# Performance work log

Measured on AMD Instinct MI355X. Metric: run time of the kernel, lower is better.

Reference implementation:

```python
import jax, jax.numpy as jnp
import numpy as np

SCALE = 1.0 / np.sqrt(512.0).astype(np.float32)  # attention() hardcodes d_k=512


def setup_inputs() -> dict:
    key = jax.random.key(0)
    ks = jax.random.split(key, 9)
    B, S, D = 4, 2048, 512
    mk = lambda k, shape: jax.random.normal(k, shape, dtype=jnp.float32) * 0.05
    return {
        "q": mk(ks[0], (B, S, D)),
        "k": mk(ks[1], (B, S, D)),
        "v": mk(ks[2], (B, S, D)),
        "WQ_w": mk(ks[3], (D, D)),
        "WQ_b": mk(ks[4], (D,)),
        "WK_w": mk(ks[5], (D, D)),
        "WK_b": mk(ks[6], (D,)),
        "WV_w": mk(ks[7], (D, D)),
        "WV_b": mk(ks[8], (D,)),
    }


def reference(q, k, v, WQ_w, WQ_b, WK_w, WK_b, WV_w, WV_b):
    # torch nn.Linear: y = x @ W.T + b
    qp = q @ WQ_w.T + WQ_b  # [B,S,dk]
    kp = k @ WK_w.T + WK_b  # [B,S,dk]
    vp = v @ WV_w.T + WV_b  # [B,S,dv]
    qk = jnp.einsum("bqd,bkd->bqk", qp, kp) * SCALE  # [B,Sq,Sk]
    S = qk.shape[1]
    tril = jnp.tril(jnp.ones((S, S), dtype=qk.dtype))  # multiplicative causal mask
    qk = qk * tril
    # NOTE: original applies softmax over dim=1 (the query axis), faithfully kept.
    attn = jax.nn.softmax(qk, axis=1)
    out = jnp.einsum("bqk,bkd->bqd", attn, vp)  # [B,Sq,dv]
    return out
```

## Files before the change

### kernel.cpp

```cpp
#include <hip/hip_runtime.h>
#include <hip/hip_bf16.h>


#define S_LEN 2048
#define D_DIM 512
#define SCALE_F 0.044194173824159216f

typedef __attribute__((ext_vector_type(8))) short s8v;
typedef __attribute__((ext_vector_type(4))) short s4v;
typedef __attribute__((ext_vector_type(4))) float f4v;

enum { EPI_BIAS = 0, EPI_BIAS_T = 1, EPI_SCORES = 2 };

__device__ __forceinline__ short f2bf_s(float f) {
  union { __hip_bfloat16 b; short s; } u; u.b = __float2bfloat16(f); return u.s;
}
__device__ __forceinline__ float bf2f_s(short h) {
  union { short s; __hip_bfloat16 b; } u; u.s = h; return __bfloat162float(u.b);
}

__device__ __forceinline__ void glds16(const short* g, short* l) {
  __builtin_amdgcn_global_load_lds((const __attribute__((address_space(1))) void*)g,
                                   (__attribute__((address_space(3))) void*)l, 16, 0, 0);
}

template <int EPI>
__device__ __forceinline__ void gemm_core(
    const short* __restrict__ A, const short* __restrict__ B,
    short* __restrict__ C, const float* __restrict__ bias,
    short* SMEM, int N, int K, size_t sCz, int m0, int n0, int bz,
    float* __restrict__ Z)
{
  short* As = SMEM;
  short* Bs = SMEM + 8192;

  const int tid  = threadIdx.x;
  const int w    = tid >> 6;
  const int lane = tid & 63;
  const int quad = lane >> 4;
  const int l16  = lane & 15;
  const int wm   = (w >> 1) * 64;
  const int wn   = (w & 1) * 64;

  const int strow = tid >> 3;
  const int gl = ((tid & 7) ^ (strow & 7)) * 8;

  f4v acc[4][4];
#pragma unroll
  for (int i = 0; i < 4; ++i)
#pragma unroll
    for (int j = 0; j < 4; ++j)
#pragma unroll
      for (int r = 0; r < 4; ++r) acc[i][j][r] = 0.0f;

  const short* Ag = A + (size_t)(m0 + strow) * K + gl;
  const short* Bg = B + (size_t)(n0 + strow) * K + gl;
  short* Asl = As + tid * 8;
  short* Bsl = Bs + tid * 8;
  const size_t pstr = (size_t)32 * K;

  const int swq = l16 & 7;

  for (int k0 = 0; k0 < K; k0 += 64) {
#pragma unroll
    for (int p = 0; p < 4; ++p) glds16(Ag + k0 + p * pstr, Asl + p * 2048);
#pragma unroll
    for (int p = 0; p < 4; ++p) glds16(Bg + k0 + p * pstr, Bsl + p * 2048);
    __syncthreads();

#pragma unroll
    for (int kk = 0; kk < 2; ++kk) {
      s8v af[4], bf[4];
#pragma unroll
      for (int i = 0; i < 4; ++i)
        af[i] = *(const s8v*)&As[(wm + i * 16 + l16) * 64 + (((kk * 4 + quad) ^ swq) * 8)];
#pragma unroll
      for (int j = 0; j < 4; ++j)
        bf[j] = *(const s8v*)&Bs[(wn + j * 16 + l16) * 64 + (((kk * 4 + quad) ^ swq) * 8)];
#pragma unroll
      for (int i = 0; i < 4; ++i)
#pragma unroll
        for (int j = 0; j < 4; ++j)
          acc[i][j] = __builtin_amdgcn_mfma_f32_16x16x32_bf16(af[i], bf[j], acc[i][j], 0, 0, 0);
    }
    __syncthreads();
  }

  float bv[4];
  if (EPI == EPI_BIAS || EPI == EPI_BIAS_T) {
#pragma unroll
    for (int j = 0; j < 4; ++j) bv[j] = bias[n0 + wn + j * 16 + l16];
  }

  if (EPI == EPI_BIAS_T) {
#pragma unroll
    for (int i = 0; i < 4; ++i) {
#pragma unroll
      for (int j = 0; j < 4; ++j) {
        const int gn  = n0 + wn + j * 16 + l16;
        const int gmb = m0 + wm + i * 16 + quad * 4;
        const int bb = gmb >> 11, ssb = gmb & (S_LEN - 1);
        s4v o;
#pragma unroll
        for (int r = 0; r < 4; ++r) o[r] = f2bf_s(acc[i][j][r] + bv[j]);
        *(s4v*)&C[((size_t)bb * D_DIM + gn) * S_LEN + ssb] = o;
      }
    }
    return;
  }

  short* TB = SMEM;
  const int wbase = w * 2176;
  float csum[4] = {0.f, 0.f, 0.f, 0.f};

#pragma unroll
  for (int ph = 0; ph < 2; ++ph) {
    __syncthreads();
#pragma unroll
    for (int ii = 0; ii < 2; ++ii) {
      const int i = ph * 2 + ii;
#pragma unroll
      for (int j = 0; j < 4; ++j) {
        const int gn = n0 + wn + j * 16 + l16;
#pragma unroll
        for (int r = 0; r < 4; ++r) {
          short o;
          if (EPI == EPI_SCORES) {
            const int gm = m0 + wm + i * 16 + quad * 4 + r;
            const float e = (gm >= gn) ? __expf(acc[i][j][r] * SCALE_F) : 1.0f;
            csum[j] += e;
            o = f2bf_s(e);
          } else {
            o = f2bf_s(acc[i][j][r] + bv[j]);
          }
          TB[wbase + (ii * 16 + quad * 4 + r) * 68 + j * 16 + l16] = o;
        }
      }
    }
    __syncthreads();
#pragma unroll
    for (int p = 0; p < 4; ++p) {
      const int row = p * 8 + (lane >> 3);
      const int cg  = lane & 7;
      const s8v vv = *(const s8v*)&TB[wbase + row * 68 + cg * 8];
      const int gm = m0 + wm + ph * 32 + row;
      const int gn = n0 + wn + cg * 8;
      *(s8v*)&C[sCz + (size_t)gm * N + gn] = vv;
    }
  }

  if (EPI == EPI_SCORES) {
#pragma unroll
    for (int j = 0; j < 4; ++j) {
      float cs = csum[j];
      cs += __shfl_xor(cs, 16, 64);
      cs += __shfl_xor(cs, 32, 64);
      if (quad == 0) atomicAdd(&Z[(bz << 11) + n0 + wn + j * 16 + l16], cs);
    }
  }
}

__global__ __launch_bounds__(256, 2) void gemm_scores(
    const short* __restrict__ A, const short* __restrict__ B, short* __restrict__ C,
    float* __restrict__ Z)
{
  __shared__ __align__(16) short SMEM[16384];
  const int bz = blockIdx.z;
  gemm_core<EPI_SCORES>(A + (size_t)bz * S_LEN * D_DIM, B + (size_t)bz * S_LEN * D_DIM,
                        C, nullptr, SMEM, S_LEN, D_DIM,
                        (size_t)bz * S_LEN * S_LEN, blockIdx.y * 128, blockIdx.x * 128,
                        bz, Z);
}

__global__ __launch_bounds__(256, 2) void proj3(
    const short* __restrict__ a0, const short* __restrict__ a1, const short* __restrict__ a2,
    const short* __restrict__ b0, const short* __restrict__ b1, const short* __restrict__ b2,
    short* __restrict__ c0, short* __restrict__ c1, short* __restrict__ c2,
    const float* __restrict__ x0, const float* __restrict__ x1, const float* __restrict__ x2)
{
  __shared__ __align__(16) short SMEM[16384];
  const int z = blockIdx.z;
  const short* A = (z == 0) ? a0 : (z == 1) ? a1 : a2;
  const short* B = (z == 0) ? b0 : (z == 1) ? b1 : b2;
  short*       C = (z == 0) ? c0 : (z == 1) ? c1 : c2;
  const float* bias = (z == 0) ? x0 : (z == 1) ? x1 : x2;
  if (z == 2)
    gemm_core<EPI_BIAS_T>(A, B, C, bias, SMEM, D_DIM, D_DIM, 0,
                          blockIdx.y * 128, blockIdx.x * 128, 0, nullptr);
  else
    gemm_core<EPI_BIAS>(A, B, C, bias, SMEM, D_DIM, D_DIM, 0,
                        blockIdx.y * 128, blockIdx.x * 128, 0, nullptr);
}

__global__ __launch_bounds__(256, 2) void gemm_out(
    const short* __restrict__ E, const short* __restrict__ vpT,
    float* __restrict__ out)
{
  __shared__ __align__(16) short As[64 * 64];
  __shared__ __align__(16) short Bs[128 * 64];

  const int tid  = threadIdx.x;
  const int bz   = blockIdx.z;
  const int m0   = blockIdx.y * 64;
  const int n0   = blockIdx.x * 128;

  const short* A = E   + (size_t)bz * S_LEN * S_LEN;
  const short* B = vpT + (size_t)bz * D_DIM * S_LEN;

  const int w    = tid >> 6;
  const int lane = tid & 63;
  const int quad = lane >> 4;
  const int l16  = lane & 15;
  const int wm   = (w >> 1) * 32;
  const int wn   = (w & 1) * 64;

  const int strow = tid >> 3;
  const int gl = ((tid & 7) ^ (strow & 7)) * 8;

  f4v acc[2][4];
#pragma unroll
  for (int i = 0; i < 2; ++i)
#pragma unroll
    for (int j = 0; j < 4; ++j)
#pragma unroll
      for (int r = 0; r < 4; ++r) acc[i][j][r] = 0.0f;

  const short* Ag = A + (size_t)(m0 + strow) * S_LEN + gl;
  const short* Bg = B + (size_t)(n0 + strow) * S_LEN + gl;
  short* Asl = As + tid * 8;
  short* Bsl = Bs + tid * 8;
  const size_t pstr = (size_t)32 * S_LEN;

  const int swq = l16 & 7;

  for (int k0 = 0; k0 < S_LEN; k0 += 64) {
#pragma unroll
    for (int p = 0; p < 2; ++p) glds16(Ag + k0 + p * pstr, Asl + p * 2048);
#pragma unroll
    for (int p = 0; p < 4; ++p) glds16(Bg + k0 + p * pstr, Bsl + p * 2048);
    __syncthreads();

#pragma unroll
    for (int kk = 0; kk < 2; ++kk) {
      s8v af[2], bf[4];
#pragma unroll
      for (int i = 0; i < 2; ++i)
        af[i] = *(const s8v*)&As[(wm + i * 16 + l16) * 64 + (((kk * 4 + quad) ^ swq) * 8)];
#pragma unroll
      for (int j = 0; j < 4; ++j)
        bf[j] = *(const s8v*)&Bs[(wn + j * 16 + l16) * 64 + (((kk * 4 + quad) ^ swq) * 8)];
#pragma unroll
      for (int i = 0; i < 2; ++i)
#pragma unroll
        for (int j = 0; j < 4; ++j)
          acc[i][j] = __builtin_amdgcn_mfma_f32_16x16x32_bf16(af[i], bf[j], acc[i][j], 0, 0, 0);
    }
    __syncthreads();
  }

  float* Cf = out + (size_t)bz * S_LEN * D_DIM;
#pragma unroll
  for (int i = 0; i < 2; ++i) {
#pragma unroll
    for (int j = 0; j < 4; ++j) {
      const int gn = n0 + wn + j * 16 + l16;
#pragma unroll
      for (int r = 0; r < 4; ++r) {
        const int gm = m0 + wm + i * 16 + quad * 4 + r;
        Cf[(size_t)gm * D_DIM + gn] = acc[i][j][r];
      }
    }
  }
}

__global__ __launch_bounds__(256) void cvt3(
    const float* __restrict__ s0, const float* __restrict__ s1,
    const float* __restrict__ s2, short* __restrict__ dst, int n)
{
  const float* s = (blockIdx.y == 0) ? s0 : (blockIdx.y == 1) ? s1 : s2;
  short* d = dst + (size_t)blockIdx.y * n;
  const int i = (blockIdx.x * 256 + threadIdx.x) * 8;
  if (i >= n) return;
  const float4 f0 = *(const float4*)(s + i);
  const float4 f1 = *(const float4*)(s + i + 4);
  s8v o;
  o[0] = f2bf_s(f0.x); o[1] = f2bf_s(f0.y); o[2] = f2bf_s(f0.z); o[3] = f2bf_s(f0.w);
  o[4] = f2bf_s(f1.x); o[5] = f2bf_s(f1.y); o[6] = f2bf_s(f1.z); o[7] = f2bf_s(f1.w);
  *(s8v*)(d + i) = o;
}

__global__ __launch_bounds__(256) void scale_vpt(
    short* __restrict__ vpT, const float* __restrict__ Z)
{
  const size_t base = ((size_t)blockIdx.x * 256 + threadIdx.x) * 8;
  const int kk = (int)(base & (S_LEN - 1));
  const int b  = (int)(base >> 20);
  const float4 z0 = *(const float4*)&Z[(b << 11) + kk];
  const float4 z1 = *(const float4*)&Z[(b << 11) + kk + 4];
  s8v v = *(s8v*)&vpT[base];
  v[0] = f2bf_s(bf2f_s(v[0]) / z0.x); v[1] = f2bf_s(bf2f_s(v[1]) / z0.y);
  v[2] = f2bf_s(bf2f_s(v[2]) / z0.z); v[3] = f2bf_s(bf2f_s(v[3]) / z0.w);
  v[4] = f2bf_s(bf2f_s(v[4]) / z1.x); v[5] = f2bf_s(bf2f_s(v[5]) / z1.y);
  v[6] = f2bf_s(bf2f_s(v[6]) / z1.z); v[7] = f2bf_s(bf2f_s(v[7]) / z1.w);
  *(s8v*)&vpT[base] = v;
}

extern "C" void kernel_launch(void* const* d_in, const int* in_sizes, int n_in,
                              void* d_out, int out_size, void* d_ws, size_t ws_size,
                              hipStream_t stream) {
  const float* q   = (const float*)d_in[0];
  const float* k   = (const float*)d_in[1];
  const float* v   = (const float*)d_in[2];
  const float* WQw = (const float*)d_in[3];
  const float* WQb = (const float*)d_in[4];
  const float* WKw = (const float*)d_in[5];
  const float* WKb = (const float*)d_in[6];
  const float* WVw = (const float*)d_in[7];
  const float* WVb = (const float*)d_in[8];

  char* ws = (char*)d_ws;
  short* E   = (short*)(ws);
  short* qb  = (short*)(ws);
  short* Wqb = (short*)(ws + 25165824);
  short* qp  = (short*)(ws + 33554432);
  short* kp  = (short*)(ws + 41943040);
  short* vpT = (short*)(ws + 50331648);
  float* Z   = (float*)(ws + 58720256);
  short* kb  = qb + 4194304;
  short* vb  = qb + 8388608;
  short* Wkb = Wqb + 262144;
  short* Wvb = Wqb + 524288;

  const dim3 blk(256);

  hipMemsetAsync(Z, 0, 4 * S_LEN * sizeof(float), stream);

  cvt3<<<dim3(2048, 3), blk, 0, stream>>>(q, k, v, qb, 4194304);
  cvt3<<<dim3(128, 3), blk, 0, stream>>>(WQw, WKw, WVw, Wqb, 262144);

  proj3<<<dim3(4, 64, 3), blk, 0, stream>>>(
      qb, kb, vb, Wqb, Wkb, Wvb, qp, kp, vpT, WQb, WKb, WVb);

  gemm_scores<<<dim3(16, 16, 4), blk, 0, stream>>>(qp, kp, E, Z);

  scale_vpt<<<dim3(2048), blk, 0, stream>>>(vpT, Z);

  gemm_out<<<dim3(4, 32, 4), blk, 0, stream>>>(E, vpT, (float*)d_out);
}
```

Before: 202.8 us.

## Multi-buffer LDS tiles to overlap global loads with MFMA in GEMM kernels

Replaces the single-buffered load/sync/compute loop with a double-buffered pipeline in the shared GEMM core (scores and projections) and a triple-buffered pipeline in the output GEMM. Loads for the next tile are issued before computing the current one, with explicit vmcnt waits and raw s_barrier in place of __syncthreads. The aim is to hide global-to-LDS latency behind MFMA work. The cost is double or more LDS per block, which can reduce occupancy, and the hand-written waitcnt counts must match the number of outstanding loads exactly.

After: 198.3 us. -2.2%, faster.

```diff
diff --git a/kernel.cpp b/kernel.cpp
--- a/kernel.cpp
+++ b/kernel.cpp
@@ -11,6 +11,9 @@
 typedef __attribute__((ext_vector_type(4))) float f4v;
 
 enum { EPI_BIAS = 0, EPI_BIAS_T = 1, EPI_SCORES = 2 };
+
+#define SBAR()    asm volatile("s_barrier" ::: "memory")
+#define WAITV(n)  asm volatile("s_waitcnt vmcnt(" #n ")" ::: "memory")
 
 __device__ __forceinline__ short f2bf_s(float f) {
   union { __hip_bfloat16 b; short s; } u; u.b = __float2bfloat16(f); return u.s;
@@ -31,9 +34,6 @@
     short* SMEM, int N, int K, size_t sCz, int m0, int n0, int bz,
     float* __restrict__ Z)
 {
-  short* As = SMEM;
-  short* Bs = SMEM + 8192;
-
   const int tid  = threadIdx.x;
   const int w    = tid >> 6;
   const int lane = tid & 63;
@@ -55,35 +55,50 @@
 
   const short* Ag = A + (size_t)(m0 + strow) * K + gl;
   const short* Bg = B + (size_t)(n0 + strow) * K + gl;
-  short* Asl = As + tid * 8;
-  short* Bsl = Bs + tid * 8;
   const size_t pstr = (size_t)32 * K;
-
+  const int t8 = tid * 8;
   const int swq = l16 & 7;
 
-  for (int k0 = 0; k0 < K; k0 += 64) {
-#pragma unroll
-    for (int p = 0; p < 4; ++p) glds16(Ag + k0 + p * pstr, Asl + p * 2048);
-#pragma unroll
-    for (int p = 0; p < 4; ++p) glds16(Bg + k0 + p * pstr, Bsl + p * 2048);
-    __syncthreads();
-
+  const int niter = K >> 6;
+
+#pragma unroll
+  for (int p = 0; p < 4; ++p) glds16(Ag + p * pstr, SMEM + t8 + p * 2048);
+#pragma unroll
+  for (int p = 0; p < 4; ++p) glds16(Bg + p * pstr, SMEM + 8192 + t8 + p * 2048);
+
+  for (int i = 0; i < niter; ++i) {
+    const int c = i & 1;
+    if (i + 1 < niter) {
+      const int k1 = (i + 1) << 6;
+      short* dA = SMEM + (1 - c) * 16384 + t8;
+#pragma unroll
+      for (int p = 0; p < 4; ++p) glds16(Ag + k1 + p * pstr, dA + p * 2048);
+#pragma unroll
+      for (int p = 0; p < 4; ++p) glds16(Bg + k1 + p * pstr, dA + 8192 + p * 2048);
+      WAITV(8);
+    } else {
+      WAITV(0);
+    }
+    SBAR();
+
+    const short* As = SMEM + c * 16384;
+    const short* Bs = As + 8192;
 #pragma unroll
     for (int kk = 0; kk < 2; ++kk) {
       s8v af[4], bf[4];
 #pragma unroll
-      for (int i = 0; i < 4; ++i)
-        af[i] = *(const s8v*)&As[(wm + i * 16 + l16) * 64 + (((kk * 4 + quad) ^ swq) * 8)];
+      for (int ii = 0; ii < 4; ++ii)
+        af[ii] = *(const s8v*)&As[(wm + ii * 16 + l16) * 64 + (((kk * 4 + quad) ^ swq) * 8)];
 #pragma unroll
       for (int j = 0; j < 4; ++j)
         bf[j] = *(const s8v*)&Bs[(wn + j * 16 + l16) * 64 + (((kk * 4 + quad) ^ swq) * 8)];
 #pragma unroll
-      for (int i = 0; i < 4; ++i)
+      for (int ii = 0; ii < 4; ++ii)
 #pragma unroll
         for (int j = 0; j < 4; ++j)
-          acc[i][j] = __builtin_amdgcn_mfma_f32_16x16x32_bf16(af[i], bf[j], acc[i][j], 0, 0, 0);
-    }
-    __syncthreads();
+          acc[ii][j] = __builtin_amdgcn_mfma_f32_16x16x32_bf16(af[ii], bf[j], acc[ii][j], 0, 0, 0);
+    }
+    SBAR();
   }
 
   float bv[4];
@@ -164,7 +179,7 @@
     const short* __restrict__ A, const short* __restrict__ B, short* __restrict__ C,
     float* __restrict__ Z)
 {
-  __shared__ __align__(16) short SMEM[16384];
+  __shared__ __align__(16) short SMEM[32768];
   const int bz = blockIdx.z;
   gemm_core<EPI_SCORES>(A + (size_t)bz * S_LEN * D_DIM, B + (size_t)bz * S_LEN * D_DIM,
                         C, nullptr, SMEM, S_LEN, D_DIM,
@@ -178,7 +193,7 @@
     short* __restrict__ c0, short* __restrict__ c1, short* __restrict__ c2,
     const float* __restrict__ x0, const float* __restrict__ x1, const float* __restrict__ x2)
 {
-  __shared__ __align__(16) short SMEM[16384];
+  __shared__ __align__(16) short SMEM[32768];
   const int z = blockIdx.z;
   const short* A = (z == 0) ? a0 : (z == 1) ? a1 : a2;
   const short* B = (z == 0) ? b0 : (z == 1) ? b1 : b2;
@@ -196,8 +211,7 @@
     const short* __restrict__ E, const short* __restrict__ vpT,
     float* __restrict__ out)
 {
-  __shared__ __align__(16) short As[64 * 64];
-  __shared__ __align__(16) short Bs[128 * 64];
+  __shared__ __align__(16) short SMEM[36864];
 
   const int tid  = threadIdx.x;
   const int bz   = blockIdx.z;
@@ -227,35 +241,59 @@
 
   const short* Ag = A + (size_t)(m0 + strow) * S_LEN + gl;
   const short* Bg = B + (size_t)(n0 + strow) * S_LEN + gl;
-  short* Asl = As + tid * 8;
-  short* Bsl = Bs + tid * 8;
   const size_t pstr = (size_t)32 * S_LEN;
-
+  const int t8 = tid * 8;
   const int swq = l16 & 7;
 
-  for (int k0 = 0; k0 < S_LEN; k0 += 64) {
-#pragma unroll
-    for (int p = 0; p < 2; ++p) glds16(Ag + k0 + p * pstr, Asl + p * 2048);
-#pragma unroll
-    for (int p = 0; p < 4; ++p) glds16(Bg + k0 + p * pstr, Bsl + p * 2048);
-    __syncthreads();
-
+  const int niter = S_LEN >> 6;
+
+#pragma unroll
+  for (int pre = 0; pre < 2; ++pre) {
+    short* dst = SMEM + pre * 12288 + t8;
+    const int k0 = pre << 6;
+#pragma unroll
+    for (int p = 0; p < 2; ++p) glds16(Ag + k0 + p * pstr, dst + p * 2048);
+#pragma unroll
+    for (int p = 0; p < 4; ++p) glds16(Bg + k0 + p * pstr, dst + 4096 + p * 2048);
+  }
+
+  int cbuf = 0, nbuf = 2;
+  for (int i = 0; i < niter; ++i) {
+    if (i + 2 < niter) {
+      const int k2 = (i + 2) << 6;
+      short* dst = SMEM + nbuf * 12288 + t8;
+#pragma unroll
+      for (int p = 0; p < 2; ++p) glds16(Ag + k2 + p * pstr, dst + p * 2048);
+#pragma unroll
+      for (int p = 0; p < 4; ++p) glds16(Bg + k2 + p * pstr, dst + 4096 + p * 2048);
+      nbuf = (nbuf == 2) ? 0 : nbuf + 1;
+      WAITV(12);
+    } else if (i + 1 < niter) {
+      WAITV(6);
+    } else {
+      WAITV(0);
+    }
+    SBAR();
+
+    const short* As = SMEM + cbuf * 12288;
+    const short* Bs = As + 4096;
+    cbuf = (cbuf == 2) ? 0 : cbuf + 1;
 #pragma unroll
     for (int kk = 0; kk < 2; ++kk) {
       s8v af[2], bf[4];
 #pragma unroll
-      for (int i = 0; i < 2; ++i)
-        af[i] = *(const s8v*)&As[(wm + i * 16 + l16) * 64 + (((kk * 4 + quad) ^ swq) * 8)];
+      for (int ii = 0; ii < 2; ++ii)
+        af[ii] = *(const s8v*)&As[(wm + ii * 16 + l16) * 64 + (((kk * 4 + quad) ^ swq) * 8)];
 #pragma unroll
       for (int j = 0; j < 4; ++j)
         bf[j] = *(const s8v*)&Bs[(wn + j * 16 + l16) * 64 + (((kk * 4 + quad) ^ swq) * 8)];
 #pragma unroll
-      for (int i = 0; i < 2; ++i)
+      for (int ii = 0; ii < 2; ++ii)
 #pragma unroll
         for (int j = 0; j < 4; ++j)
-          acc[i][j] = __builtin_amdgcn_mfma_f32_16x16x32_bf16(af[i], bf[j], acc[i][j], 0, 0, 0);
-    }
-    __syncthreads();
+          acc[ii][j] = __builtin_amdgcn_mfma_f32_16x16x32_bf16(af[ii], bf[j], acc[ii][j], 0, 0, 0);
+    }
+    SBAR();
   }
 
   float* Cf = out + (size_t)bz * S_LEN * D_DIM;
```
